# Performance work log

Measured on AMD Instinct MI355X. Metric: run time of the kernel, lower is better.

## Reference

```python
import jax, jax.numpy as jnp
import numpy as np

B, T, C = 8, 2048, 1024
HS, HO = 64, 64  # head_size, head_output_dim

def setup_inputs() -> dict:
    key = jax.random.key(0)
    k1, k2, k3, k4 = jax.random.split(key, 4)
    x = jax.random.normal(k1, (B, T, C), dtype=jnp.float32)
    Wk = jax.random.normal(k2, (HS, C), dtype=jnp.float32) * (C ** -0.5)
    Wq = jax.random.normal(k3, (HS, C), dtype=jnp.float32) * (C ** -0.5)
    Wv = jax.random.normal(k4, (HO, C), dtype=jnp.float32) * (C ** -0.5)
    return {"x": x, "Wk": Wk, "Wq": Wq, "Wv": Wv}

def reference(x, Wk, Wq, Wv):
    Bx, Tx, Cx = x.shape
    k = jnp.einsum('btc,hc->bth', x, Wk)  # [B,T,HS]
    q = jnp.einsum('btc,hc->bth', x, Wq)  # [B,T,HS]
    v = jnp.einsum('btc,oc->bto', x, Wv)  # [B,T,HO]
    scores = jnp.einsum('bth,bsh->bts', q, k)  # [B,T,T]
    causal = jnp.tril(jnp.ones((Tx, Tx), dtype=bool))
    scores = jnp.where(causal, scores, -jnp.inf)
    # original scales AFTER masking; -inf * scale stays -inf, same softmax result
    weights = jax.nn.softmax(scores * (HS ** -0.5), axis=-1)
    return jnp.einsum('bts,bso->bto', weights, v)
```

## Files before the change

kernel.cpp:

```cpp
#include <hip/hip_runtime.h>
#include <hip/hip_bf16.h>

typedef __attribute__((ext_vector_type(8))) short short8;
typedef __attribute__((ext_vector_type(4))) float float4v;

#define LOG2E 1.44269504088896340736f

typedef __attribute__((address_space(1))) const unsigned int gu32;
typedef __attribute__((address_space(3))) unsigned int su32;

__device__ __forceinline__ unsigned short f2bf(float f) {
    unsigned int u = __float_as_uint(f);
    unsigned int r = (u + 0x7fffu + ((u >> 16) & 1u)) >> 16;
    return (unsigned short)r;
}

__global__ void wconv_kernel(const float* __restrict__ Wk, const float* __restrict__ Wq,
                             const float* __restrict__ Wv, unsigned short* __restrict__ Wb) {
    int i = blockIdx.x * 256 + threadIdx.x;
    if (i >= 192 * 1024) return;
    float v;
    if (i < 65536)       v = Wk[i];
    else if (i < 131072) v = Wq[i - 65536];
    else                 v = Wv[i - 131072];
    Wb[i] = f2bf(v);
}

__global__ __launch_bounds__(256) void proj_kernel(
    const float* __restrict__ x, const unsigned short* __restrict__ Wb,
    unsigned short* __restrict__ qs, unsigned short* __restrict__ ks,
    unsigned short* __restrict__ vT) {
    __shared__ unsigned short Bl[2][12288];

    const int tid  = threadIdx.x;
    const int lane = tid & 63;
    const int wave = tid >> 6;
    const int rg   = wave & 1;
    const int g    = wave >> 1;
    const int quad = lane >> 4;
    const int l16  = lane & 15;
    const int t0   = blockIdx.x * 32;

    const int srow_in = lane >> 3;
    const int csrc    = (lane & 7) ^ srow_in;

    const int rowA = t0 + rg * 16 + l16;
    const float* xr = x + (size_t)rowA * 1024;

    float4v acc[6];
#pragma unroll
    for (int n = 0; n < 6; n++) acc[n] = (float4v){0.f, 0.f, 0.f, 0.f};

#define STAGE_B(BUF, KN)                                                          \
    {                                                                             \
        _Pragma("unroll")                                                         \
        for (int i = 0; i < 6; i++) {                                             \
            const int region = wave * 6 + i;                                      \
            const int rowg   = region * 8 + srow_in;                              \
            const unsigned short* src = Wb + (size_t)rowg * 1024 + (KN) + csrc * 8; \
            __builtin_amdgcn_global_load_lds((gu32*)src,                          \
                                             (su32*)&Bl[BUF][region * 512],       \
                                             16, 0, 0);                           \
        }                                                                         \
    }

    STAGE_B(0, 0)
    float4v a0[4], a1[4];
    a0[0] = *(const float4v*)(xr + quad * 8);
    a0[1] = *(const float4v*)(xr + quad * 8 + 4);
    a0[2] = *(const float4v*)(xr + 32 + quad * 8);
    a0[3] = *(const float4v*)(xr + 32 + quad * 8 + 4);
    a1[0] = *(const float4v*)(xr + 64 + quad * 8);
    a1[1] = *(const float4v*)(xr + 64 + quad * 8 + 4);
    a1[2] = *(const float4v*)(xr + 96 + quad * 8);
    a1[3] = *(const float4v*)(xr + 96 + quad * 8 + 4);

    const int swz = l16 & 7;

#pragma unroll
    for (int kt = 0; kt < 16; kt++) {
        __builtin_amdgcn_sched_barrier(0);
        if (kt < 15) {
            asm volatile("s_waitcnt vmcnt(4)" ::: "memory");
        } else {
            asm volatile("s_waitcnt vmcnt(0)" ::: "memory");
        }
        __builtin_amdgcn_s_barrier();
        if (kt < 15) STAGE_B((kt + 1) & 1, (kt + 1) * 64)
        asm volatile("" ::: "memory");
        float4v an[4];
        if (kt < 14) {
            const int kn2 = (kt + 2) * 64;
            an[0] = *(const float4v*)(xr + kn2 + quad * 8);
            an[1] = *(const float4v*)(xr + kn2 + quad * 8 + 4);
            an[2] = *(const float4v*)(xr + kn2 + 32 + quad * 8);
            an[3] = *(const float4v*)(xr + kn2 + 32 + quad * 8 + 4);
        }
        const unsigned short* Bc = Bl[kt & 1];
#pragma unroll
        for (int kc = 0; kc < 2; kc++) {
            short8 af;
#pragma unroll
            for (int j = 0; j < 4; j++) af[j] = (short)f2bf(a0[kc * 2][j]);
#pragma unroll
            for (int j = 0; j < 4; j++) af[4 + j] = (short)f2bf(a0[kc * 2 + 1][j]);
#pragma unroll
            for (int n = 0; n < 6; n++) {
                const int row  = (g * 6 + n) * 16 + l16;
                const int coff = ((kc * 4 + quad) ^ swz) * 8;
                const short8 bf = *(const short8*)&Bc[row * 64 + coff];
                acc[n] = __builtin_amdgcn_mfma_f32_16x16x32_bf16(af, bf, acc[n], 0, 0, 0);
            }
        }
        if (kt < 14) {
#pragma unroll
            for (int i = 0; i < 4; i++) { a0[i] = a1[i]; a1[i] = an[i]; }
        } else if (kt < 15) {
#pragma unroll
            for (int i = 0; i < 4; i++) a0[i] = a1[i];
        }
    }
#undef STAGE_B

    const int rowD = t0 + rg * 16 + quad * 4;
#pragma unroll
    for (int r = 0; r < 4; r++) {
        const int t = rowD + r;
        const int b = t >> 11, tt = t & 2047;
        if (g == 0) {
#pragma unroll
            for (int n = 0; n < 4; n++)
                ks[(size_t)t * 64 + n * 16 + l16] = f2bf(acc[n][r]);
#pragma unroll
            for (int n = 4; n < 6; n++)
                qs[(size_t)t * 64 + (n - 4) * 16 + l16] = f2bf(acc[n][r] * 0.125f);
        } else {
#pragma unroll
            for (int n = 0; n < 2; n++)
                qs[(size_t)t * 64 + (n + 2) * 16 + l16] = f2bf(acc[n][r] * 0.125f);
#pragma unroll
            for (int n = 2; n < 6; n++)
                vT[(size_t)b * 131072 + (size_t)((n - 2) * 16 + l16) * 2048 + tt] = f2bf(acc[n][r]);
        }
    }
}

__global__ __launch_bounds__(256) void attn_kernel(
    const unsigned short* __restrict__ qs, const unsigned short* __restrict__ ks,
    const unsigned short* __restrict__ vT, float* __restrict__ out) {
    __shared__ unsigned short Kl[4 * 64 * 72];
    __shared__ unsigned short Vl[64 * 264];
    __shared__ unsigned short P[4][16 * 72];
    __shared__ float Ll[4][16];
    float* Of = (float*)Kl;

    const int tid  = threadIdx.x;
    const int lane = tid & 63;
    const int wave = tid >> 6;
    const int quad = lane >> 4;
    const int l16  = lane & 15;
    const int bx   = blockIdx.x;
    const int b    = bx & 7;
    const int i    = bx >> 3;
    const int qt   = (i & 1) ? (127 - (i >> 1)) : (i >> 1);
    const int t0   = qt * 16;

    const unsigned short* qb = qs + (size_t)b * 131072;
    const unsigned short* kb = ks + (size_t)b * 131072;
    const unsigned short* vb = vT + (size_t)b * 131072;

    const int ksr = tid >> 3;
    const int ksc = (tid & 7) * 8;
    const int vsr = tid >> 5;
    const int vsc = (tid & 31) * 8;

    const int qrow = t0 + l16;
    const short8 qf0 = *(const short8*)(qb + (size_t)qrow * 64 + quad * 8);
    const short8 qf1 = *(const short8*)(qb + (size_t)qrow * 64 + 32 + quad * 8);

    float4v o[4];
#pragma unroll
    for (int ot = 0; ot < 4; ot++) o[ot] = (float4v){0.f, 0.f, 0.f, 0.f};
    float lpart = 0.f;

    const int nkb  = (qt >> 2) + 1;
    const int nsup = (nkb + 3) >> 2;

    for (int s = 0; s < nsup; s++) {
        const int key0 = s * 256;
        __syncthreads();
#pragma unroll
        for (int i2 = 0; i2 < 8; i2++) {
            int kr = key0 + i2 * 32 + ksr; kr = kr < 2047 ? kr : 2047;
            *(short8*)&Kl[(i2 * 32 + ksr) * 72 + ksc] = *(const short8*)(kb + (size_t)kr * 64 + ksc);
        }
#pragma unroll
        for (int i2 = 0; i2 < 8; i2++) {
            const int orow = i2 * 8 + vsr;
            int kc2 = key0 + vsc; kc2 = kc2 < 2040 ? kc2 : 2040;
            *(short8*)&Vl[orow * 264 + vsc] = *(const short8*)(vb + (size_t)orow * 2048 + kc2);
        }
        __syncthreads();

        const int jt = s * 4 + wave;
        if (jt < nkb) {
            const int kbase = wave * 64;
            float4v sv[4];
#pragma unroll
            for (int kt = 0; kt < 4; kt++) {
                const short8 ka = *(const short8*)&Kl[(kbase + kt * 16 + l16) * 72 + quad * 8];
                const short8 kc = *(const short8*)&Kl[(kbase + kt * 16 + l16) * 72 + 32 + quad * 8];
                float4v z = (float4v){0.f, 0.f, 0.f, 0.f};
                z = __builtin_amdgcn_mfma_f32_16x16x32_bf16(ka, qf0, z, 0, 0, 0);
                sv[kt] = __builtin_amdgcn_mfma_f32_16x16x32_bf16(kc, qf1, z, 0, 0, 0);
            }
            if (jt == nkb - 1) {
#pragma unroll
                for (int kt = 0; kt < 4; kt++)
#pragma unroll
                    for (int r = 0; r < 4; r++)
                        if (jt * 64 + kt * 16 + quad * 4 + r > qrow) sv[kt][r] = -1e30f;
            }
#pragma unroll
            for (int kt = 0; kt < 4; kt++) {
                float p0 = exp2f(sv[kt][0] * LOG2E);
                float p1 = exp2f(sv[kt][1] * LOG2E);
                float p2 = exp2f(sv[kt][2] * LOG2E);
                float p3 = exp2f(sv[kt][3] * LOG2E);
                lpart += (p0 + p1) + (p2 + p3);
                unsigned int lo = (unsigned int)f2bf(p0) | ((unsigned int)f2bf(p1) << 16);
                unsigned int hi = (unsigned int)f2bf(p2) | ((unsigned int)f2bf(p3) << 16);
                unsigned long long w = ((unsigned long long)hi << 32) | lo;
                *(unsigned long long*)&P[wave][l16 * 72 + kt * 16 + quad * 4] = w;
            }
#pragma unroll
            for (int kc = 0; kc < 2; kc++) {
                const short8 pf = *(const short8*)&P[wave][l16 * 72 + kc * 32 + quad * 8];
#pragma unroll
                for (int ot = 0; ot < 4; ot++) {
                    const short8 vf = *(const short8*)&Vl[(ot * 16 + l16) * 264 + wave * 64 + kc * 32 + quad * 8];
                    o[ot] = __builtin_amdgcn_mfma_f32_16x16x32_bf16(pf, vf, o[ot], 0, 0, 0);
                }
            }
        }
    }

    lpart += __shfl_xor(lpart, 16);
    lpart += __shfl_xor(lpart, 32);
    __syncthreads();
#pragma unroll
    for (int r = 0; r < 4; r++)
#pragma unroll
        for (int ot = 0; ot < 4; ot++)
            Of[wave * 1088 + (quad * 4 + r) * 68 + ot * 16 + l16] = o[ot][r];
    if (lane < 16) Ll[wave][lane] = lpart;
    __syncthreads();

    {
        const int row = tid >> 4;
        const int c0  = (tid & 15) * 4;
        const float lsum = Ll[0][row] + Ll[1][row] + Ll[2][row] + Ll[3][row];
        float4v v0 = *(const float4v*)&Of[0 * 1088 + row * 68 + c0];
        float4v v1 = *(const float4v*)&Of[1 * 1088 + row * 68 + c0];
        float4v v2 = *(const float4v*)&Of[2 * 1088 + row * 68 + c0];
        float4v v3 = *(const float4v*)&Of[3 * 1088 + row * 68 + c0];
        float4v res;
        const float inv = 1.0f / lsum;
#pragma unroll
        for (int j = 0; j < 4; j++)
            res[j] = ((v0[j] + v1[j]) + (v2[j] + v3[j])) * inv;
        float* ob = out + (size_t)b * 131072 + (size_t)(t0 + row) * 64 + c0;
        *(float4v*)ob = res;
    }
}

extern "C" void kernel_launch(void* const* d_in, const int* in_sizes, int n_in,
                              void* d_out, int out_size, void* d_ws, size_t ws_size,
                              hipStream_t stream) {
    const float* x  = (const float*)d_in[0];
    const float* Wk = (const float*)d_in[1];
    const float* Wq = (const float*)d_in[2];
    const float* Wv = (const float*)d_in[3];
    float* out = (float*)d_out;

    unsigned short* Wb  = (unsigned short*)d_ws;
    unsigned short* qsb = (unsigned short*)((char*)d_ws + 393216);
    unsigned short* ksb = qsb + 1048576;
    unsigned short* vTb = ksb + 1048576;

    hipLaunchKernelGGL(wconv_kernel, dim3(768), dim3(256), 0, stream, Wk, Wq, Wv, Wb);
    hipLaunchKernelGGL(proj_kernel, dim3(512), dim3(256), 0, stream, x, Wb, qsb, ksb, vTb);
    hipLaunchKernelGGL(attn_kernel, dim3(1024), dim3(256), 0, stream, qsb, ksb, vTb, out);
}
```

Measured before the change: 150.0 us.

## Retile projection waves so each owns its staged weight rows and drop barriers

In the projection kernel, each wave now computes both 16-row token groups against 48 output columns, instead of one row group against 96 columns. That 48-column slice is exactly the set of weight rows the wave stages into LDS itself. Because no wave reads another wave's staged weights, the per-iteration workgroup barrier and sched barrier are removed, and the vmcnt wait is raised to match the larger number of outstanding x loads. Each LDS weight fragment now feeds two MFMAs. The trade-off is that every wave loads and converts x for all 32 rows, which doubles global x reads and fp32-to-bf16 conversion work.

```diff
diff --git a/kernel.cpp b/kernel.cpp
--- a/kernel.cpp
+++ b/kernel.cpp
@@ -35,8 +35,6 @@
     const int tid  = threadIdx.x;
     const int lane = tid & 63;
     const int wave = tid >> 6;
-    const int rg   = wave & 1;
-    const int g    = wave >> 1;
     const int quad = lane >> 4;
     const int l16  = lane & 15;
     const int t0   = blockIdx.x * 32;
@@ -44,12 +42,14 @@
     const int srow_in = lane >> 3;
     const int csrc    = (lane & 7) ^ srow_in;
 
-    const int rowA = t0 + rg * 16 + l16;
-    const float* xr = x + (size_t)rowA * 1024;
-
-    float4v acc[6];
-#pragma unroll
-    for (int n = 0; n < 6; n++) acc[n] = (float4v){0.f, 0.f, 0.f, 0.f};
+    const float* xr0 = x + (size_t)(t0 + l16) * 1024;
+    const float* xr1 = x + (size_t)(t0 + 16 + l16) * 1024;
+
+    float4v acc[3][2];
+#pragma unroll
+    for (int nn = 0; nn < 3; nn++)
+#pragma unroll
+        for (int m = 0; m < 2; m++) acc[nn][m] = (float4v){0.f, 0.f, 0.f, 0.f};
 
 #define STAGE_B(BUF, KN)                                                          \
     {                                                                             \
@@ -64,83 +64,89 @@
         }                                                                         \
     }
 
+#define LOAD_A(DST, KN)                                        \
+    {                                                          \
+        DST[0] = *(const float4v*)(xr0 + (KN) + quad * 8);     \
+        DST[1] = *(const float4v*)(xr0 + (KN) + quad * 8 + 4); \
+        DST[2] = *(const float4v*)(xr0 + (KN) + 32 + quad * 8);     \
+        DST[3] = *(const float4v*)(xr0 + (KN) + 32 + quad * 8 + 4); \
+        DST[4] = *(const float4v*)(xr1 + (KN) + quad * 8);     \
+        DST[5] = *(const float4v*)(xr1 + (KN) + quad * 8 + 4); \
+        DST[6] = *(const float4v*)(xr1 + (KN) + 32 + quad * 8);     \
+        DST[7] = *(const float4v*)(xr1 + (KN) + 32 + quad * 8 + 4); \
+    }
+
     STAGE_B(0, 0)
-    float4v a0[4], a1[4];
-    a0[0] = *(const float4v*)(xr + quad * 8);
-    a0[1] = *(const float4v*)(xr + quad * 8 + 4);
-    a0[2] = *(const float4v*)(xr + 32 + quad * 8);
-    a0[3] = *(const float4v*)(xr + 32 + quad * 8 + 4);
-    a1[0] = *(const float4v*)(xr + 64 + quad * 8);
-    a1[1] = *(const float4v*)(xr + 64 + quad * 8 + 4);
-    a1[2] = *(const float4v*)(xr + 96 + quad * 8);
-    a1[3] = *(const float4v*)(xr + 96 + quad * 8 + 4);
+    asm volatile("" ::: "memory");
+    float4v a0[8], a1[8];
+    LOAD_A(a0, 0)
+    LOAD_A(a1, 64)
 
     const int swz = l16 & 7;
 
 #pragma unroll
     for (int kt = 0; kt < 16; kt++) {
-        __builtin_amdgcn_sched_barrier(0);
         if (kt < 15) {
-            asm volatile("s_waitcnt vmcnt(4)" ::: "memory");
+            asm volatile("s_waitcnt vmcnt(8)" ::: "memory");
         } else {
             asm volatile("s_waitcnt vmcnt(0)" ::: "memory");
         }
-        __builtin_amdgcn_s_barrier();
         if (kt < 15) STAGE_B((kt + 1) & 1, (kt + 1) * 64)
         asm volatile("" ::: "memory");
-        float4v an[4];
+        float4v an[8];
+        if (kt < 14) LOAD_A(an, (kt + 2) * 64)
+
+        const unsigned short* Bc = Bl[kt & 1];
+#pragma unroll
+        for (int kc = 0; kc < 2; kc++) {
+            short8 af0, af1;
+#pragma unroll
+            for (int j = 0; j < 4; j++) af0[j] = (short)f2bf(a0[kc * 2][j]);
+#pragma unroll
+            for (int j = 0; j < 4; j++) af0[4 + j] = (short)f2bf(a0[kc * 2 + 1][j]);
+#pragma unroll
+            for (int j = 0; j < 4; j++) af1[j] = (short)f2bf(a0[4 + kc * 2][j]);
+#pragma unroll
+            for (int j = 0; j < 4; j++) af1[4 + j] = (short)f2bf(a0[4 + kc * 2 + 1][j]);
+            const int coff = ((kc * 4 + quad) ^ swz) * 8;
+#pragma unroll
+            for (int nn = 0; nn < 3; nn++) {
+                const int row = wave * 48 + nn * 16 + l16;
+                const short8 bf = *(const short8*)&Bc[row * 64 + coff];
+                acc[nn][0] = __builtin_amdgcn_mfma_f32_16x16x32_bf16(af0, bf, acc[nn][0], 0, 0, 0);
+                acc[nn][1] = __builtin_amdgcn_mfma_f32_16x16x32_bf16(af1, bf, acc[nn][1], 0, 0, 0);
+            }
+        }
         if (kt < 14) {
-            const int kn2 = (kt + 2) * 64;
-            an[0] = *(const float4v*)(xr + kn2 + quad * 8);
-            an[1] = *(const float4v*)(xr + kn2 + quad * 8 + 4);
-            an[2] = *(const float4v*)(xr + kn2 + 32 + quad * 8);
-            an[3] = *(const float4v*)(xr + kn2 + 32 + quad * 8 + 4);
-        }
-        const unsigned short* Bc = Bl[kt & 1];
-#pragma unroll
-        for (int kc = 0; kc < 2; kc++) {
-            short8 af;
-#pragma unroll
-            for (int j = 0; j < 4; j++) af[j] = (short)f2bf(a0[kc * 2][j]);
-#pragma unroll
-            for (int j = 0; j < 4; j++) af[4 + j] = (short)f2bf(a0[kc * 2 + 1][j]);
-#pragma unroll
-            for (int n = 0; n < 6; n++) {
-                const int row  = (g * 6 + n) * 16 + l16;
-                const int coff = ((kc * 4 + quad) ^ swz) * 8;
-                const short8 bf = *(const short8*)&Bc[row * 64 + coff];
-                acc[n] = __builtin_amdgcn_mfma_f32_16x16x32_bf16(af, bf, acc[n], 0, 0, 0);
-            }
-        }
-        if (kt < 14) {
-#pragma unroll
-            for (int i = 0; i < 4; i++) { a0[i] = a1[i]; a1[i] = an[i]; }
+#pragma unroll
+            for (int i = 0; i < 8; i++) { a0[i] = a1[i]; a1[i] = an[i]; }
         } else if (kt < 15) {
 #pragma unroll
-            for (int i = 0; i < 4; i++) a0[i] = a1[i];
+            for (int i = 0; i < 8; i++) a0[i] = a1[i];
         }
     }
 #undef STAGE_B
-
-    const int rowD = t0 + rg * 16 + quad * 4;
-#pragma unroll
-    for (int r = 0; r < 4; r++) {
-        const int t = rowD + r;
-        const int b = t >> 11, tt = t & 2047;
-        if (g == 0) {
-#pragma unroll
-            for (int n = 0; n < 4; n++)
-                ks[(size_t)t * 64 + n * 16 + l16] = f2bf(acc[n][r]);
-#pragma unroll
-            for (int n = 4; n < 6; n++)
-                qs[(size_t)t * 64 + (n - 4) * 16 + l16] = f2bf(acc[n][r] * 0.125f);
-        } else {
-#pragma unroll
-            for (int n = 0; n < 2; n++)
-                qs[(size_t)t * 64 + (n + 2) * 16 + l16] = f2bf(acc[n][r] * 0.125f);
-#pragma unroll
-            for (int n = 2; n < 6; n++)
-                vT[(size_t)b * 131072 + (size_t)((n - 2) * 16 + l16) * 2048 + tt] = f2bf(acc[n][r]);
+#undef LOAD_A
+
+    const int rowD = t0 + quad * 4;
+#pragma unroll
+    for (int m = 0; m < 2; m++) {
+#pragma unroll
+        for (int nn = 0; nn < 3; nn++) {
+            const int mt = wave * 3 + nn;
+#pragma unroll
+            for (int r = 0; r < 4; r++) {
+                const int t = rowD + m * 16 + r;
+                const float val = acc[nn][m][r];
+                if (mt < 4) {
+                    ks[(size_t)t * 64 + mt * 16 + l16] = f2bf(val);
+                } else if (mt < 8) {
+                    qs[(size_t)t * 64 + (mt - 4) * 16 + l16] = f2bf(val * 0.125f);
+                } else {
+                    const int b = t >> 11, tt = t & 2047;
+                    vT[(size_t)b * 131072 + (size_t)((mt - 8) * 16 + l16) * 2048 + tt] = f2bf(val);
+                }
+            }
         }
     }
 }
```

Result: slower. 162.7 us (+8.5%).

## Load K and V fragments directly from global memory, dropping LDS staging

Applied to the files above, without the earlier changes.

Each wave now reads its K rows and transposed V columns straight from global memory into MFMA fragments. This replaces the cooperative block-wide staging into shared memory and the two barriers per 256-key super-block. It also shrinks shared memory to the P scratch and output-reduction buffers and adds a min-blocks-per-CU launch bound to raise occupancy. The cost is uncoalesced 16-byte global loads that rely on L2/L1 hits, and waves no longer share staged data.

```diff
diff --git a/kernel.cpp b/kernel.cpp
--- a/kernel.cpp
+++ b/kernel.cpp
@@ -145,14 +145,12 @@
     }
 }
 
-__global__ __launch_bounds__(256) void attn_kernel(
+__global__ __launch_bounds__(256, 4) void attn_kernel(
     const unsigned short* __restrict__ qs, const unsigned short* __restrict__ ks,
     const unsigned short* __restrict__ vT, float* __restrict__ out) {
-    __shared__ unsigned short Kl[4 * 64 * 72];
-    __shared__ unsigned short Vl[64 * 264];
     __shared__ unsigned short P[4][16 * 72];
     __shared__ float Ll[4][16];
-    float* Of = (float*)Kl;
+    __shared__ float Of[4][16][68];
 
     const int tid  = threadIdx.x;
     const int lane = tid & 63;
@@ -169,11 +167,6 @@
     const unsigned short* kb = ks + (size_t)b * 131072;
     const unsigned short* vb = vT + (size_t)b * 131072;
 
-    const int ksr = tid >> 3;
-    const int ksc = (tid & 7) * 8;
-    const int vsr = tid >> 5;
-    const int vsc = (tid & 31) * 8;
-
     const int qrow = t0 + l16;
     const short8 qf0 = *(const short8*)(qb + (size_t)qrow * 64 + quad * 8);
     const short8 qf1 = *(const short8*)(qb + (size_t)qrow * 64 + 32 + quad * 8);
@@ -183,64 +176,46 @@
     for (int ot = 0; ot < 4; ot++) o[ot] = (float4v){0.f, 0.f, 0.f, 0.f};
     float lpart = 0.f;
 
-    const int nkb  = (qt >> 2) + 1;
-    const int nsup = (nkb + 3) >> 2;
-
-    for (int s = 0; s < nsup; s++) {
-        const int key0 = s * 256;
-        __syncthreads();
-#pragma unroll
-        for (int i2 = 0; i2 < 8; i2++) {
-            int kr = key0 + i2 * 32 + ksr; kr = kr < 2047 ? kr : 2047;
-            *(short8*)&Kl[(i2 * 32 + ksr) * 72 + ksc] = *(const short8*)(kb + (size_t)kr * 64 + ksc);
-        }
-#pragma unroll
-        for (int i2 = 0; i2 < 8; i2++) {
-            const int orow = i2 * 8 + vsr;
-            int kc2 = key0 + vsc; kc2 = kc2 < 2040 ? kc2 : 2040;
-            *(short8*)&Vl[orow * 264 + vsc] = *(const short8*)(vb + (size_t)orow * 2048 + kc2);
-        }
-        __syncthreads();
-
-        const int jt = s * 4 + wave;
-        if (jt < nkb) {
-            const int kbase = wave * 64;
-            float4v sv[4];
-#pragma unroll
-            for (int kt = 0; kt < 4; kt++) {
-                const short8 ka = *(const short8*)&Kl[(kbase + kt * 16 + l16) * 72 + quad * 8];
-                const short8 kc = *(const short8*)&Kl[(kbase + kt * 16 + l16) * 72 + 32 + quad * 8];
-                float4v z = (float4v){0.f, 0.f, 0.f, 0.f};
-                z = __builtin_amdgcn_mfma_f32_16x16x32_bf16(ka, qf0, z, 0, 0, 0);
-                sv[kt] = __builtin_amdgcn_mfma_f32_16x16x32_bf16(kc, qf1, z, 0, 0, 0);
-            }
-            if (jt == nkb - 1) {
-#pragma unroll
-                for (int kt = 0; kt < 4; kt++)
-#pragma unroll
-                    for (int r = 0; r < 4; r++)
-                        if (jt * 64 + kt * 16 + quad * 4 + r > qrow) sv[kt][r] = -1e30f;
-            }
-#pragma unroll
-            for (int kt = 0; kt < 4; kt++) {
-                float p0 = exp2f(sv[kt][0] * LOG2E);
-                float p1 = exp2f(sv[kt][1] * LOG2E);
-                float p2 = exp2f(sv[kt][2] * LOG2E);
-                float p3 = exp2f(sv[kt][3] * LOG2E);
-                lpart += (p0 + p1) + (p2 + p3);
-                unsigned int lo = (unsigned int)f2bf(p0) | ((unsigned int)f2bf(p1) << 16);
-                unsigned int hi = (unsigned int)f2bf(p2) | ((unsigned int)f2bf(p3) << 16);
-                unsigned long long w = ((unsigned long long)hi << 32) | lo;
-                *(unsigned long long*)&P[wave][l16 * 72 + kt * 16 + quad * 4] = w;
-            }
-#pragma unroll
-            for (int kc = 0; kc < 2; kc++) {
-                const short8 pf = *(const short8*)&P[wave][l16 * 72 + kc * 32 + quad * 8];
-#pragma unroll
-                for (int ot = 0; ot < 4; ot++) {
-                    const short8 vf = *(const short8*)&Vl[(ot * 16 + l16) * 264 + wave * 64 + kc * 32 + quad * 8];
-                    o[ot] = __builtin_amdgcn_mfma_f32_16x16x32_bf16(pf, vf, o[ot], 0, 0, 0);
-                }
+    const int nkb = (qt >> 2) + 1;
+
+    for (int jt = wave; jt < nkb; jt += 4) {
+        const unsigned short* krow = kb + (size_t)jt * 64 * 64;
+        float4v sv[4];
+#pragma unroll
+        for (int kt = 0; kt < 4; kt++) {
+            const short8 ka = *(const short8*)(krow + (size_t)(kt * 16 + l16) * 64 + quad * 8);
+            const short8 kc = *(const short8*)(krow + (size_t)(kt * 16 + l16) * 64 + 32 + quad * 8);
+            float4v z = (float4v){0.f, 0.f, 0.f, 0.f};
+            z = __builtin_amdgcn_mfma_f32_16x16x32_bf16(ka, qf0, z, 0, 0, 0);
+            sv[kt] = __builtin_amdgcn_mfma_f32_16x16x32_bf16(kc, qf1, z, 0, 0, 0);
+        }
+        if (jt == nkb - 1) {
+#pragma unroll
+            for (int kt = 0; kt < 4; kt++)
+#pragma unroll
+                for (int r = 0; r < 4; r++)
+                    if (jt * 64 + kt * 16 + quad * 4 + r > qrow) sv[kt][r] = -1e30f;
+        }
+#pragma unroll
+        for (int kt = 0; kt < 4; kt++) {
+            float p0 = exp2f(sv[kt][0] * LOG2E);
+            float p1 = exp2f(sv[kt][1] * LOG2E);
+            float p2 = exp2f(sv[kt][2] * LOG2E);
+            float p3 = exp2f(sv[kt][3] * LOG2E);
+            lpart += (p0 + p1) + (p2 + p3);
+            unsigned int lo = (unsigned int)f2bf(p0) | ((unsigned int)f2bf(p1) << 16);
+            unsigned int hi = (unsigned int)f2bf(p2) | ((unsigned int)f2bf(p3) << 16);
+            unsigned long long w = ((unsigned long long)hi << 32) | lo;
+            *(unsigned long long*)&P[wave][l16 * 72 + kt * 16 + quad * 4] = w;
+        }
+#pragma unroll
+        for (int kc = 0; kc < 2; kc++) {
+            const short8 pf = *(const short8*)&P[wave][l16 * 72 + kc * 32 + quad * 8];
+#pragma unroll
+            for (int ot = 0; ot < 4; ot++) {
+                const short8 vf = *(const short8*)(vb + (size_t)(ot * 16 + l16) * 2048
+                                                  + jt * 64 + kc * 32 + quad * 8);
+                o[ot] = __builtin_amdgcn_mfma_f32_16x16x32_bf16(pf, vf, o[ot], 0, 0, 0);
             }
         }
     }
@@ -252,7 +227,7 @@
     for (int r = 0; r < 4; r++)
 #pragma unroll
         for (int ot = 0; ot < 4; ot++)
-            Of[wave * 1088 + (quad * 4 + r) * 68 + ot * 16 + l16] = o[ot][r];
+            Of[wave][quad * 4 + r][ot * 16 + l16] = o[ot][r];
     if (lane < 16) Ll[wave][lane] = lpart;
     __syncthreads();
 
@@ -260,10 +235,10 @@
         const int row = tid >> 4;
         const int c0  = (tid & 15) * 4;
         const float lsum = Ll[0][row] + Ll[1][row] + Ll[2][row] + Ll[3][row];
-        float4v v0 = *(const float4v*)&Of[0 * 1088 + row * 68 + c0];
-        float4v v1 = *(const float4v*)&Of[1 * 1088 + row * 68 + c0];
-        float4v v2 = *(const float4v*)&Of[2 * 1088 + row * 68 + c0];
-        float4v v3 = *(const float4v*)&Of[3 * 1088 + row * 68 + c0];
+        float4v v0 = *(const float4v*)&Of[0][row][c0];
+        float4v v1 = *(const float4v*)&Of[1][row][c0];
+        float4v v2 = *(const float4v*)&Of[2][row][c0];
+        float4v v3 = *(const float4v*)&Of[3][row][c0];
         float4v res;
         const float inv = 1.0f / lsum;
 #pragma unroll
```

New measurement: 168.3 us. +12.2%, slower.

## Fuse weight bf16 conversion into projection kernel via register-staged loads

Applied to the files above, without the earlier changes.

Removes the separate weight-conversion kernel launch. The projection kernel now loads fp32 weights directly into registers, converts them to bf16 and writes them to LDS. The direct global-to-LDS async loads are replaced by register staging, with the wait and barrier moved to after the MFMA work so loads overlap compute. In exchange, every block re-reads and re-converts the fp32 weights, which doubles weight traffic per block and raises register pressure.

```diff
diff --git a/kernel.cpp b/kernel.cpp
--- a/kernel.cpp
+++ b/kernel.cpp
@@ -5,9 +5,6 @@
 typedef __attribute__((ext_vector_type(4))) float float4v;
 
 #define LOG2E 1.44269504088896340736f
-
-typedef __attribute__((address_space(1))) const unsigned int gu32;
-typedef __attribute__((address_space(3))) unsigned int su32;
 
 __device__ __forceinline__ unsigned short f2bf(float f) {
     unsigned int u = __float_as_uint(f);
@@ -15,19 +12,9 @@
     return (unsigned short)r;
 }
 
-__global__ void wconv_kernel(const float* __restrict__ Wk, const float* __restrict__ Wq,
-                             const float* __restrict__ Wv, unsigned short* __restrict__ Wb) {
-    int i = blockIdx.x * 256 + threadIdx.x;
-    if (i >= 192 * 1024) return;
-    float v;
-    if (i < 65536)       v = Wk[i];
-    else if (i < 131072) v = Wq[i - 65536];
-    else                 v = Wv[i - 131072];
-    Wb[i] = f2bf(v);
-}
-
 __global__ __launch_bounds__(256) void proj_kernel(
-    const float* __restrict__ x, const unsigned short* __restrict__ Wb,
+    const float* __restrict__ x, const float* __restrict__ Wk,
+    const float* __restrict__ Wq, const float* __restrict__ Wv,
     unsigned short* __restrict__ qs, unsigned short* __restrict__ ks,
     unsigned short* __restrict__ vT) {
     __shared__ unsigned short Bl[2][12288];
@@ -42,7 +29,17 @@
     const int t0   = blockIdx.x * 32;
 
     const int srow_in = lane >> 3;
-    const int csrc    = (lane & 7) ^ srow_in;
+    const int schunk  = lane & 7;
+    const int wchunk  = schunk ^ srow_in;
+
+    const float* wrow[6];
+#pragma unroll
+    for (int i = 0; i < 6; i++) {
+        const int rowg = (wave * 6 + i) * 8 + srow_in;
+        wrow[i] = (rowg < 64)  ? (Wk + (size_t)rowg * 1024)
+                : (rowg < 128) ? (Wq + (size_t)(rowg - 64) * 1024)
+                               : (Wv + (size_t)(rowg - 128) * 1024);
+    }
 
     const int rowA = t0 + rg * 16 + l16;
     const float* xr = x + (size_t)rowA * 1024;
@@ -51,51 +48,59 @@
 #pragma unroll
     for (int n = 0; n < 6; n++) acc[n] = (float4v){0.f, 0.f, 0.f, 0.f};
 
-#define STAGE_B(BUF, KN)                                                          \
-    {                                                                             \
-        _Pragma("unroll")                                                         \
-        for (int i = 0; i < 6; i++) {                                             \
-            const int region = wave * 6 + i;                                      \
-            const int rowg   = region * 8 + srow_in;                              \
-            const unsigned short* src = Wb + (size_t)rowg * 1024 + (KN) + csrc * 8; \
-            __builtin_amdgcn_global_load_lds((gu32*)src,                          \
-                                             (su32*)&Bl[BUF][region * 512],       \
-                                             16, 0, 0);                           \
-        }                                                                         \
-    }
-
-    STAGE_B(0, 0)
+#define STAGE_LOAD(REG, KN)                                                   \
+    {                                                                         \
+        _Pragma("unroll")                                                     \
+        for (int i = 0; i < 6; i++) {                                         \
+            const float* src = wrow[i] + (KN) + schunk * 8;                   \
+            REG[i * 2]     = *(const float4v*)(src);                          \
+            REG[i * 2 + 1] = *(const float4v*)(src + 4);                      \
+        }                                                                     \
+    }
+
+#define STAGE_WRITE(BUF, REG)                                                 \
+    {                                                                         \
+        _Pragma("unroll")                                                     \
+        for (int i = 0; i < 6; i++) {                                         \
+            short8 w;                                                         \
+            _Pragma("unroll")                                                 \
+            for (int j = 0; j < 4; j++) {                                     \
+                w[j]     = (short)f2bf(REG[i * 2][j]);                        \
+                w[4 + j] = (short)f2bf(REG[i * 2 + 1][j]);                    \
+            }                                                                 \
+            *(short8*)&Bl[BUF][(wave * 6 + i) * 512 + srow_in * 64 + wchunk * 8] = w; \
+        }                                                                     \
+    }
+
+#define LOAD_A(DST, KN)                                             \
+    {                                                               \
+        DST[0] = *(const float4v*)(xr + (KN) + quad * 8);           \
+        DST[1] = *(const float4v*)(xr + (KN) + quad * 8 + 4);       \
+        DST[2] = *(const float4v*)(xr + (KN) + 32 + quad * 8);      \
+        DST[3] = *(const float4v*)(xr + (KN) + 32 + quad * 8 + 4);  \
+    }
+
+    float4v breg[12];
     float4v a0[4], a1[4];
-    a0[0] = *(const float4v*)(xr + quad * 8);
-    a0[1] = *(const float4v*)(xr + quad * 8 + 4);
-    a0[2] = *(const float4v*)(xr + 32 + quad * 8);
-    a0[3] = *(const float4v*)(xr + 32 + quad * 8 + 4);
-    a1[0] = *(const float4v*)(xr + 64 + quad * 8);
-    a1[1] = *(const float4v*)(xr + 64 + quad * 8 + 4);
-    a1[2] = *(const float4v*)(xr + 96 + quad * 8);
-    a1[3] = *(const float4v*)(xr + 96 + quad * 8 + 4);
+    STAGE_LOAD(breg, 0)
+    asm volatile("" ::: "memory");
+    LOAD_A(a0, 0)
+    LOAD_A(a1, 64)
+    asm volatile("s_waitcnt vmcnt(4)" ::: "memory");
+    STAGE_WRITE(0, breg)
+    asm volatile("s_waitcnt lgkmcnt(0)" ::: "memory");
+    __builtin_amdgcn_s_barrier();
 
     const int swz = l16 & 7;
 
 #pragma unroll
     for (int kt = 0; kt < 16; kt++) {
-        __builtin_amdgcn_sched_barrier(0);
-        if (kt < 15) {
-            asm volatile("s_waitcnt vmcnt(4)" ::: "memory");
-        } else {
-            asm volatile("s_waitcnt vmcnt(0)" ::: "memory");
-        }
-        __builtin_amdgcn_s_barrier();
-        if (kt < 15) STAGE_B((kt + 1) & 1, (kt + 1) * 64)
+        if (kt < 15) STAGE_LOAD(breg, (kt + 1) * 64)
         asm volatile("" ::: "memory");
         float4v an[4];
-        if (kt < 14) {
-            const int kn2 = (kt + 2) * 64;
-            an[0] = *(const float4v*)(xr + kn2 + quad * 8);
-            an[1] = *(const float4v*)(xr + kn2 + quad * 8 + 4);
-            an[2] = *(const float4v*)(xr + kn2 + 32 + quad * 8);
-            an[3] = *(const float4v*)(xr + kn2 + 32 + quad * 8 + 4);
-        }
+        if (kt < 14) LOAD_A(an, (kt + 2) * 64)
+        asm volatile("" ::: "memory");
+
         const unsigned short* Bc = Bl[kt & 1];
 #pragma unroll
         for (int kc = 0; kc < 2; kc++) {
@@ -112,6 +117,18 @@
                 acc[n] = __builtin_amdgcn_mfma_f32_16x16x32_bf16(af, bf, acc[n], 0, 0, 0);
             }
         }
+
+        if (kt < 15) {
+            if (kt < 14) {
+                asm volatile("s_waitcnt vmcnt(4)" ::: "memory");
+            } else {
+                asm volatile("s_waitcnt vmcnt(0)" ::: "memory");
+            }
+            STAGE_WRITE((kt + 1) & 1, breg)
+            asm volatile("s_waitcnt lgkmcnt(0)" ::: "memory");
+            __builtin_amdgcn_s_barrier();
+        }
+
         if (kt < 14) {
 #pragma unroll
             for (int i = 0; i < 4; i++) { a0[i] = a1[i]; a1[i] = an[i]; }
@@ -120,7 +137,9 @@
             for (int i = 0; i < 4; i++) a0[i] = a1[i];
         }
     }
-#undef STAGE_B
+#undef STAGE_LOAD
+#undef STAGE_WRITE
+#undef LOAD_A
 
     const int rowD = t0 + rg * 16 + quad * 4;
 #pragma unroll
@@ -283,12 +302,10 @@
     const float* Wv = (const float*)d_in[3];
     float* out = (float*)d_out;
 
-    unsigned short* Wb  = (unsigned short*)d_ws;
     unsigned short* qsb = (unsigned short*)((char*)d_ws + 393216);
     unsigned short* ksb = qsb + 1048576;
     unsigned short* vTb = ksb + 1048576;
 
-    hipLaunchKernelGGL(wconv_kernel, dim3(768), dim3(256), 0, stream, Wk, Wq, Wv, Wb);
-    hipLaunchKernelGGL(proj_kernel, dim3(512), dim3(256), 0, stream, x, Wb, qsb, ksb, vTb);
+    hipLaunchKernelGGL(proj_kernel, dim3(512), dim3(256), 0, stream, x, Wk, Wq, Wv, qsb, ksb, vTb);
     hipLaunchKernelGGL(attn_kernel, dim3(1024), dim3(256), 0, stream, qsb, ksb, vTb, out);
 }
```

Measured after the change: 154.6 us. 1.03x slower.
